# Kernel tuning notes

Hardware: AMD Instinct MI355X
Metric: run time of the kernel (lower is better)

## Reference

```python
import jax, jax.numpy as jnp
import numpy as np

B, L, R = 4, 2048, 1024        # batch, seq_len, residual_dim
HID, EXP, K = 64, 2, 3          # hidden_dim, expansion_factor, conv_kernel_size
D = HID * EXP                   # ssm_input_dim = 128
N = HID                         # SSM state size = 64


def setup_inputs() -> dict:
    key = jax.random.key(0)
    ks = jax.random.split(key, 16)
    g = lambda k, s: jax.random.normal(k, s, dtype=jnp.float32) * 0.02
    inp = {
        "up_x":   jax.random.normal(ks[0], (B, L, R), dtype=jnp.float32),
        "W_up":   g(ks[1], (R, 2 * D)),
        "b_up":   g(ks[2], (2 * D,)),
        "conv_w": g(ks[3], (D, K)),          # depthwise Conv1d weight [C,1,K] squeezed
        "conv_b": g(ks[4], (D,)),
        "W_delta": g(ks[5], (D, D)),
        "b_delta": g(ks[6], (D,)),
        "W_B":    g(ks[7], (D, N)),
        "b_B":    g(ks[8], (N,)),
        "W_C":    g(ks[9], (D, N)),
        "b_C":    g(ks[10], (N,)),
        "A_log":  jnp.log(jnp.broadcast_to(jnp.arange(1, N + 1, dtype=jnp.float32), (D, N))),
        "D_skip": jnp.ones((D,), dtype=jnp.float32),
        "W_down": g(ks[11], (D, R)),
        "b_down": g(ks[12], (R,)),
    }
    return inp


def reference(up_x, W_up, b_up, conv_w, conv_b, W_delta, b_delta,
              W_B, b_B, W_C, b_C, A_log, D_skip, W_down, b_down):
    Lq = up_x.shape[1]
    u = up_x @ W_up + b_up                               # [B,L,2D]
    left, right = jnp.split(u, 2, axis=-1)               # each [B,L,D]

    # causal depthwise conv (pad left K-1, truncate to L)
    xp = jnp.pad(left, ((0, 0), (K - 1, 0), (0, 0)))     # [B,L+K-1,D]
    conv = sum(conv_w[:, k] * xp[:, k:k + Lq, :] for k in range(K)) + conv_b
    x = jax.nn.silu(conv)                                # [B,L,D]

    # S6 selective scan
    delta = jax.nn.softplus(x @ W_delta + b_delta)       # [B,L,D]
    Bm = x @ W_B + b_B                                   # [B,L,N]
    Cm = x @ W_C + b_C                                   # [B,L,N]
    A = -jnp.exp(A_log)                                  # [D,N]
    dA = jnp.exp(delta[..., None] * A)                   # [B,L,D,N]
    dBx = delta[..., None] * Bm[:, :, None, :] * x[..., None]  # [B,L,D,N]

    def step(h, inputs):
        dA_t, dBx_t, C_t = inputs                        # [B,D,N],[B,D,N],[B,N]
        h = dA_t * h + dBx_t
        y_t = jnp.einsum('bdn,bn->bd', h, C_t)
        return h, y_t

    h0 = jnp.zeros((up_x.shape[0], D, N), dtype=x.dtype)
    _, ys = jax.lax.scan(step, h0, (jnp.swapaxes(dA, 0, 1),
                                    jnp.swapaxes(dBx, 0, 1),
                                    jnp.swapaxes(Cm, 0, 1)))
    y = jnp.swapaxes(ys, 0, 1) + D_skip * x              # [B,L,D]

    gated = y * jax.nn.silu(right)                       # SiLU gate
    return gated @ W_down + b_down                       # [B,L,R]
```

## Files before the change

### kernel.cpp

```cpp
#include <hip/hip_runtime.h>
#include <math.h>

#define B_ 4
#define L_ 2048
#define R_ 1024
#define D_ 128
#define N_ 64
#define TWO_D 256
#define M_ (B_*L_)

#define LNC 6
#define NC 64

#define LSTR 68
#define LSTRX 136

typedef __attribute__((ext_vector_type(8))) short bf16x8;
typedef __attribute__((ext_vector_type(4))) float f32x4;
typedef __attribute__((ext_vector_type(4))) unsigned short u16x4;

__device__ __forceinline__ float silu_f(float z) {
    return z * __builtin_amdgcn_rcpf(1.0f + __expf(-z));
}

__device__ __forceinline__ float softplus_f(float z) {
    return fmaxf(z, 0.0f) + __logf(1.0f + __expf(-fabsf(z)));
}

__device__ __forceinline__ short f2bf(float f) {
    union { float f; unsigned int u; } v; v.f = f;
    unsigned int r = v.u + 0x7FFF + ((v.u >> 16) & 1);
    return (short)(r >> 16);
}

__device__ __forceinline__ float bf2f(unsigned short s) {
    union { float f; unsigned int u; } v;
    v.u = ((unsigned int)s) << 16;
    return v.f;
}

__device__ __forceinline__ bf16x8 pack8(float4 a, float4 b) {
    bf16x8 r;
    r[0] = f2bf(a.x); r[1] = f2bf(a.y); r[2] = f2bf(a.z); r[3] = f2bf(a.w);
    r[4] = f2bf(b.x); r[5] = f2bf(b.y); r[6] = f2bf(b.z); r[7] = f2bf(b.w);
    return r;
}

__global__ __launch_bounds__(256) void gemm_up_splitk(
    const float* __restrict__ A,
    const float* __restrict__ W,
    float* __restrict__ P0,
    float* __restrict__ P1)
{
    __shared__ short Al[128 * LSTR];
    __shared__ short Bl[64 * LSTR];

    int lid = blockIdx.x;
    int xcd = lid & 7;
    int slot = lid >> 3;
    int bm = xcd * 8 + (slot >> 3);
    int r3 = slot & 7;
    int bn = r3 & 3;
    int split = r3 >> 2;
    float* P = split ? P1 : P0;
    int k0 = split * 512;

    int tid = threadIdx.x;
    int w = tid >> 6, l = tid & 63;
    int lm = l & 15, q = l >> 4;
    int wm = w * 32;

    f32x4 acc[2][4];
    #pragma unroll
    for (int i = 0; i < 2; i++)
        #pragma unroll
        for (int f = 0; f < 4; f++)
            acc[i][f] = (f32x4){0.f, 0.f, 0.f, 0.f};

    int ar = tid >> 1, ak = (tid & 1) * 16;
    int bcol = tid & 63, bk = (tid >> 6) * 8;

    const float* Ag = A + (size_t)(bm * 128 + ar) * 1024 + k0 + ak;
    const float* Wg = W + (size_t)k0 * TWO_D + (size_t)bn * 64 + bcol;

    for (int kt = 0; kt < 512; kt += 32) {
        float4 a0 = *(const float4*)(Ag + kt);
        float4 a1 = *(const float4*)(Ag + kt + 4);
        float4 a2 = *(const float4*)(Ag + kt + 8);
        float4 a3 = *(const float4*)(Ag + kt + 12);
        *(bf16x8*)&Al[ar * LSTR + ak]     = pack8(a0, a1);
        *(bf16x8*)&Al[ar * LSTR + ak + 8] = pack8(a2, a3);

        float w0 = Wg[(size_t)(kt + bk + 0) * TWO_D];
        float w1 = Wg[(size_t)(kt + bk + 1) * TWO_D];
        float w2 = Wg[(size_t)(kt + bk + 2) * TWO_D];
        float w3 = Wg[(size_t)(kt + bk + 3) * TWO_D];
        float w4 = Wg[(size_t)(kt + bk + 4) * TWO_D];
        float w5 = Wg[(size_t)(kt + bk + 5) * TWO_D];
        float w6 = Wg[(size_t)(kt + bk + 6) * TWO_D];
        float w7 = Wg[(size_t)(kt + bk + 7) * TWO_D];
        *(bf16x8*)&Bl[bcol * LSTR + bk] =
            pack8(make_float4(w0, w1, w2, w3), make_float4(w4, w5, w6, w7));

        __syncthreads();

        bf16x8 af0 = *(bf16x8*)&Al[(wm + lm) * LSTR + q * 8];
        bf16x8 af1 = *(bf16x8*)&Al[(wm + 16 + lm) * LSTR + q * 8];
        bf16x8 bfr[4];
        #pragma unroll
        for (int f = 0; f < 4; f++)
            bfr[f] = *(bf16x8*)&Bl[(f * 16 + lm) * LSTR + q * 8];

        #pragma unroll
        for (int f = 0; f < 4; f++) {
            acc[0][f] = __builtin_amdgcn_mfma_f32_16x16x32_bf16(af0, bfr[f], acc[0][f], 0, 0, 0);
            acc[1][f] = __builtin_amdgcn_mfma_f32_16x16x32_bf16(af1, bfr[f], acc[1][f], 0, 0, 0);
        }

        __syncthreads();
    }

    #pragma unroll
    for (int i = 0; i < 2; i++)
        #pragma unroll
        for (int f = 0; f < 4; f++)
            #pragma unroll
            for (int e = 0; e < 4; e++) {
                int row = bm * 128 + wm + i * 16 + q * 4 + e;
                int col = bn * 64 + f * 16 + lm;
                P[(size_t)row * TWO_D + col] = acc[i][f][e];
            }
}

__global__ __launch_bounds__(256) void convproj_mfma(
    const float* __restrict__ P0,
    const float* __restrict__ P1,
    const float* __restrict__ b_up,
    const float* __restrict__ conv_w,
    const float* __restrict__ conv_b,
    const float* __restrict__ W_delta, const float* __restrict__ b_delta,
    const float* __restrict__ W_B,     const float* __restrict__ b_B,
    const float* __restrict__ W_C,     const float* __restrict__ b_C,
    unsigned short* __restrict__ x,
    float* __restrict__ u,
    unsigned short* __restrict__ delta,
    unsigned short* __restrict__ Bm,
    unsigned short* __restrict__ Cm)
{
    __shared__ float uu[66 * 128];
    __shared__ short Xl[64 * LSTRX];
    __shared__ short Bl[64 * LSTR];

    int lid = blockIdx.x;
    int xcd = lid & 7;
    int slot = lid >> 3;
    int bm = xcd * 16 + (slot >> 2);
    int bn = slot & 3;
    int tid = threadIdx.x;

    bool seq_start = (bm & 31) == 0;

    #pragma unroll
    for (int i = 0; i < 9; i++) {
        int fi = tid + i * 256;
        if (fi < 2112) {
            int row = fi >> 5;
            int c4 = (fi & 31) * 4;
            int gr = bm * 64 + row - 2;
            float4 v;
            if (seq_start && row < 2) {
                v = make_float4(0.f, 0.f, 0.f, 0.f);
            } else {
                size_t gi = (size_t)gr * TWO_D + c4;
                float4 p0 = *(const float4*)&P0[gi];
                float4 p1 = *(const float4*)&P1[gi];
                float4 bb = *(const float4*)&b_up[c4];
                v = make_float4(p0.x + p1.x + bb.x, p0.y + p1.y + bb.y,
                                p0.z + p1.z + bb.z, p0.w + p1.w + bb.w);
            }
            *(float4*)&uu[fi * 4] = v;
        }
    }

    if (bn == 1) {
        #pragma unroll
        for (int i = 0; i < 8; i++) {
            int fi = tid + i * 256;
            int row = fi >> 5;
            int c4 = (fi & 31) * 4 + 128;
            int gr = bm * 64 + row;
            size_t gi = (size_t)gr * TWO_D + c4;
            float4 p0 = *(const float4*)&P0[gi];
            float4 p1 = *(const float4*)&P1[gi];
            float4 bb = *(const float4*)&b_up[c4];
            *(float4*)&u[gi] = make_float4(p0.x + p1.x + bb.x, p0.y + p1.y + bb.y,
                                           p0.z + p1.z + bb.z, p0.w + p1.w + bb.w);
        }
    }
    __syncthreads();

    #pragma unroll
    for (int i = 0; i < 8; i++) {
        int fi = tid + i * 256;
        int row = fi >> 5;
        int c4 = (fi & 31) * 4;
        float4 v2 = *(const float4*)&uu[(row + 2) * 128 + c4];
        float4 v1 = *(const float4*)&uu[(row + 1) * 128 + c4];
        float4 v0 = *(const float4*)&uu[(row + 0) * 128 + c4];
        float4 z;
        {
            float w0 = conv_w[(c4 + 0) * 3 + 0], w1 = conv_w[(c4 + 0) * 3 + 1], w2 = conv_w[(c4 + 0) * 3 + 2];
            z.x = silu_f(fmaf(w0, v0.x, fmaf(w1, v1.x, fmaf(w2, v2.x, conv_b[c4 + 0]))));
        }
        {
            float w0 = conv_w[(c4 + 1) * 3 + 0], w1 = conv_w[(c4 + 1) * 3 + 1], w2 = conv_w[(c4 + 1) * 3 + 2];
            z.y = silu_f(fmaf(w0, v0.y, fmaf(w1, v1.y, fmaf(w2, v2.y, conv_b[c4 + 1]))));
        }
        {
            float w0 = conv_w[(c4 + 2) * 3 + 0], w1 = conv_w[(c4 + 2) * 3 + 1], w2 = conv_w[(c4 + 2) * 3 + 2];
            z.z = silu_f(fmaf(w0, v0.z, fmaf(w1, v1.z, fmaf(w2, v2.z, conv_b[c4 + 2]))));
        }
        {
            float w0 = conv_w[(c4 + 3) * 3 + 0], w1 = conv_w[(c4 + 3) * 3 + 1], w2 = conv_w[(c4 + 3) * 3 + 2];
            z.w = silu_f(fmaf(w0, v0.w, fmaf(w1, v1.w, fmaf(w2, v2.w, conv_b[c4 + 3]))));
        }
        short4 zb;
        zb.x = f2bf(z.x); zb.y = f2bf(z.y); zb.z = f2bf(z.z); zb.w = f2bf(z.w);
        *(short4*)&Xl[row * LSTRX + c4] = zb;
        if (bn == 0) {
            int gr = bm * 64 + row;
            *(short4*)&x[(size_t)gr * D_ + c4] = zb;
        }
    }

    const float* Wsel; const float* bsel; int wstride;
    if (bn < 2)       { Wsel = W_delta + bn * 64; bsel = b_delta + bn * 64; wstride = 128; }
    else if (bn == 2) { Wsel = W_B;               bsel = b_B;               wstride = 64;  }
    else              { Wsel = W_C;               bsel = b_C;               wstride = 64;  }

    int w = tid >> 6, l = tid & 63;
    int lm = l & 15, q = l >> 4;
    int wm = (w & 1) * 32, wn = (w >> 1) * 32;

    f32x4 acc00 = {0,0,0,0}, acc01 = {0,0,0,0}, acc10 = {0,0,0,0}, acc11 = {0,0,0,0};

    int bcol = tid & 63, bk = (tid >> 6) * 8;
    const float* Wg = Wsel + bcol;

    __syncthreads();

    for (int kt = 0; kt < 128; kt += 32) {
        float w0 = Wg[(size_t)(kt + bk + 0) * wstride];
        float w1 = Wg[(size_t)(kt + bk + 1) * wstride];
        float w2 = Wg[(size_t)(kt + bk + 2) * wstride];
        float w3 = Wg[(size_t)(kt + bk + 3) * wstride];
        float w4 = Wg[(size_t)(kt + bk + 4) * wstride];
        float w5 = Wg[(size_t)(kt + bk + 5) * wstride];
        float w6 = Wg[(size_t)(kt + bk + 6) * wstride];
        float w7 = Wg[(size_t)(kt + bk + 7) * wstride];
        *(bf16x8*)&Bl[bcol * LSTR + bk] =
            pack8(make_float4(w0, w1, w2, w3), make_float4(w4, w5, w6, w7));

        __syncthreads();

        bf16x8 af0 = *(bf16x8*)&Xl[(wm + lm) * LSTRX + kt + q * 8];
        bf16x8 af1 = *(bf16x8*)&Xl[(wm + 16 + lm) * LSTRX + kt + q * 8];
        bf16x8 bf0 = *(bf16x8*)&Bl[(wn + lm) * LSTR + q * 8];
        bf16x8 bf1 = *(bf16x8*)&Bl[(wn + 16 + lm) * LSTR + q * 8];

        acc00 = __builtin_amdgcn_mfma_f32_16x16x32_bf16(af0, bf0, acc00, 0, 0, 0);
        acc01 = __builtin_amdgcn_mfma_f32_16x16x32_bf16(af0, bf1, acc01, 0, 0, 0);
        acc10 = __builtin_amdgcn_mfma_f32_16x16x32_bf16(af1, bf0, acc10, 0, 0, 0);
        acc11 = __builtin_amdgcn_mfma_f32_16x16x32_bf16(af1, bf1, acc11, 0, 0, 0);

        __syncthreads();
    }

    #pragma unroll
    for (int i = 0; i < 4; i++) {
        int r0 = bm * 64 + wm + q * 4 + i;
        int r1 = r0 + 16;
        int c0 = wn + lm;
        int c1 = c0 + 16;
        float v00 = acc00[i] + bsel[c0];
        float v01 = acc01[i] + bsel[c1];
        float v10 = acc10[i] + bsel[c0];
        float v11 = acc11[i] + bsel[c1];
        if (bn < 2) {
            int cc0 = bn * 64 + c0, cc1 = bn * 64 + c1;
            delta[(size_t)r0 * D_ + cc0] = (unsigned short)f2bf(softplus_f(v00));
            delta[(size_t)r0 * D_ + cc1] = (unsigned short)f2bf(softplus_f(v01));
            delta[(size_t)r1 * D_ + cc0] = (unsigned short)f2bf(softplus_f(v10));
            delta[(size_t)r1 * D_ + cc1] = (unsigned short)f2bf(softplus_f(v11));
        } else if (bn == 2) {
            Bm[(size_t)r0 * N_ + c0] = (unsigned short)f2bf(v00);
            Bm[(size_t)r0 * N_ + c1] = (unsigned short)f2bf(v01);
            Bm[(size_t)r1 * N_ + c0] = (unsigned short)f2bf(v10);
            Bm[(size_t)r1 * N_ + c1] = (unsigned short)f2bf(v11);
        } else {
            Cm[(size_t)r0 * N_ + c0] = (unsigned short)f2bf(v00);
            Cm[(size_t)r0 * N_ + c1] = (unsigned short)f2bf(v01);
            Cm[(size_t)r1 * N_ + c0] = (unsigned short)f2bf(v10);
            Cm[(size_t)r1 * N_ + c1] = (unsigned short)f2bf(v11);
        }
    }
}

__global__ __launch_bounds__(256) void scan_sumA(
    const unsigned short* __restrict__ delta,
    const unsigned short* __restrict__ x,
    const unsigned short* __restrict__ Bm,
    const float* __restrict__ A_log,
    float* __restrict__ ch_aprod,
    float* __restrict__ ch_h)
{
    constexpr int TCt = L_ >> LNC;
    __shared__ unsigned short ld_d[TCt * 16];
    __shared__ unsigned short ld_x[TCt * 16];
    __shared__ unsigned short ld_b[TCt * 64];

    int blk = blockIdx.x;
    int c = blk & (NC - 1);
    int dqg = (blk >> LNC) & 7;
    int b = blk >> (LNC + 3);
    int tid = threadIdx.x;
    int wv = tid >> 6;
    int l = tid & 63;
    int g = l >> 4, j = l & 15;
    int d0 = dqg * 16;
    int d = d0 + wv * 4 + g;
    int dloc = wv * 4 + g;

    size_t row0 = (size_t)b * L_ + c * TCt;

    {
        int t = (tid & 127) >> 2;
        int c4 = (tid & 3) * 4;
        const unsigned short* src = (tid < 128) ? delta : x;
        unsigned short* dst = (tid < 128) ? ld_d : ld_x;
        *(u16x4*)&dst[t * 16 + c4] = *(const u16x4*)&src[(row0 + t) * D_ + d0 + c4];
    }
    {
        int t = tid >> 3;
        int c8 = (tid & 7) * 8;
        *(bf16x8*)&ld_b[t * 64 + c8] = *(const bf16x8*)&Bm[(row0 + t) * N_ + c8];
    }

    const float LOG2E = 1.44269504089f;
    float4 Ar = *(const float4*)&A_log[d * N_ + j * 4];
    float Ai0 = -__expf(Ar.x) * LOG2E;
    float Ai1 = -__expf(Ar.y) * LOG2E;
    float Ai2 = -__expf(Ar.z) * LOG2E;
    float Ai3 = -__expf(Ar.w) * LOG2E;

    __syncthreads();

    float h0 = 0, h1 = 0, h2 = 0, h3 = 0;
    float S = 0;

    #pragma unroll 8
    for (int t = 0; t < TCt; t++) {
        float dl = bf2f(ld_d[t * 16 + dloc]);
        float xv = bf2f(ld_x[t * 16 + dloc]);
        u16x4 bv = *(const u16x4*)&ld_b[t * 64 + j * 4];
        float e0 = exp2f(dl * Ai0);
        float e1 = exp2f(dl * Ai1);
        float e2 = exp2f(dl * Ai2);
        float e3 = exp2f(dl * Ai3);
        float dbx = dl * xv;
        h0 = fmaf(e0, h0, dbx * bf2f(bv[0]));
        h1 = fmaf(e1, h1, dbx * bf2f(bv[1]));
        h2 = fmaf(e2, h2, dbx * bf2f(bv[2]));
        h3 = fmaf(e3, h3, dbx * bf2f(bv[3]));
        S += dl;
    }

    size_t ci = (((size_t)b * D_ + d) * NC + c) * N_ + j * 4;
    *(float4*)&ch_aprod[ci] = make_float4(exp2f(Ai0 * S), exp2f(Ai1 * S),
                                          exp2f(Ai2 * S), exp2f(Ai3 * S));
    *(float4*)&ch_h[ci]     = make_float4(h0, h1, h2, h3);
}

__global__ __launch_bounds__(64) void scan_prefix(
    float* __restrict__ aprod_hin,
    const float* __restrict__ ch_h)
{
    int idx = blockIdx.x * 64 + threadIdx.x;
    int n = idx & 63;
    int rest = idx >> 6;
    size_t base = (size_t)rest * NC * N_ + n;
    float h = 0.0f;
    #pragma unroll 8
    for (int c = 0; c < NC; c++) {
        size_t o = base + (size_t)c * N_;
        float a  = aprod_hin[o];
        float hh = ch_h[o];
        aprod_hin[o] = h;
        h = fmaf(a, h, hh);
    }
}

__global__ __launch_bounds__(256) void scan_outB(
    const unsigned short* __restrict__ delta,
    const unsigned short* __restrict__ x,
    const unsigned short* __restrict__ Bm,
    const unsigned short* __restrict__ Cm,
    const float* __restrict__ A_log,
    const float* __restrict__ D_skip,
    const float* __restrict__ hin,
    const float* __restrict__ u,
    short* __restrict__ gated)
{
    constexpr int TCt = L_ >> LNC;
    __shared__ unsigned short ld_d[TCt * 16];
    __shared__ unsigned short ld_x[TCt * 16];
    __shared__ unsigned short ld_b[TCt * 64];
    __shared__ unsigned short ld_c[TCt * 64];
    __shared__ float yl[TCt * 16];

    int blk = blockIdx.x;
    int c = blk & (NC - 1);
    int dqg = (blk >> LNC) & 7;
    int b = blk >> (LNC + 3);
    int tid = threadIdx.x;
    int wv = tid >> 6;
    int l = tid & 63;
    int g = l >> 4, j = l & 15;
    int d0 = dqg * 16;
    int d = d0 + wv * 4 + g;
    int dloc = wv * 4 + g;

    size_t row0 = (size_t)b * L_ + c * TCt;

    {
        int t = (tid & 127) >> 2;
        int c4 = (tid & 3) * 4;
        const unsigned short* src = (tid < 128) ? delta : x;
        unsigned short* dst = (tid < 128) ? ld_d : ld_x;
        *(u16x4*)&dst[t * 16 + c4] = *(const u16x4*)&src[(row0 + t) * D_ + d0 + c4];
    }
    {
        int t = tid >> 3;
        int c8 = (tid & 7) * 8;
        *(bf16x8*)&ld_b[t * 64 + c8] = *(const bf16x8*)&Bm[(row0 + t) * N_ + c8];
        *(bf16x8*)&ld_c[t * 64 + c8] = *(const bf16x8*)&Cm[(row0 + t) * N_ + c8];
    }

    const float LOG2E = 1.44269504089f;
    float4 Ar = *(const float4*)&A_log[d * N_ + j * 4];
    float Ai0 = -__expf(Ar.x) * LOG2E;
    float Ai1 = -__expf(Ar.y) * LOG2E;
    float Ai2 = -__expf(Ar.z) * LOG2E;
    float Ai3 = -__expf(Ar.w) * LOG2E;
    float dsk = D_skip[d];

    float4 hv = *(const float4*)&hin[(((size_t)b * D_ + d) * NC + c) * N_ + j * 4];
    float h0 = hv.x, h1 = hv.y, h2 = hv.z, h3 = hv.w;

    __syncthreads();

    #pragma unroll 8
    for (int t = 0; t < TCt; t++) {
        float dl = bf2f(ld_d[t * 16 + dloc]);
        float xv = bf2f(ld_x[t * 16 + dloc]);
        u16x4 bv = *(const u16x4*)&ld_b[t * 64 + j * 4];
        u16x4 cv = *(const u16x4*)&ld_c[t * 64 + j * 4];
        float e0 = exp2f(dl * Ai0);
        float e1 = exp2f(dl * Ai1);
        float e2 = exp2f(dl * Ai2);
        float e3 = exp2f(dl * Ai3);
        float dbx = dl * xv;
        h0 = fmaf(e0, h0, dbx * bf2f(bv[0]));
        h1 = fmaf(e1, h1, dbx * bf2f(bv[1]));
        h2 = fmaf(e2, h2, dbx * bf2f(bv[2]));
        h3 = fmaf(e3, h3, dbx * bf2f(bv[3]));
        float p = fmaf(h0, bf2f(cv[0]), fmaf(h1, bf2f(cv[1]),
                  fmaf(h2, bf2f(cv[2]), h3 * bf2f(cv[3]))));
        p += __shfl_xor(p, 1, 64);
        p += __shfl_xor(p, 2, 64);
        p += __shfl_xor(p, 4, 64);
        p += __shfl_xor(p, 8, 64);
        if (j == 0) yl[t * 16 + dloc] = fmaf(dsk, xv, p);
    }

    __syncthreads();

    if (tid < 128) {
        int t = tid >> 2;
        int c4 = (tid & 3) * 4;
        size_t row = row0 + t;
        float4 yv = *(float4*)&yl[t * 16 + c4];
        float4 gv = *(const float4*)&u[row * TWO_D + 128 + d0 + c4];
        short4 o;
        o.x = f2bf(yv.x * silu_f(gv.x));
        o.y = f2bf(yv.y * silu_f(gv.y));
        o.z = f2bf(yv.z * silu_f(gv.z));
        o.w = f2bf(yv.w * silu_f(gv.w));
        *(short4*)&gated[row * D_ + d0 + c4] = o;
    }
}

__global__ __launch_bounds__(256) void gemm_down_mfma(
    const short* __restrict__ gated,
    const float* __restrict__ W,
    const float* __restrict__ bias,
    float* __restrict__ out)
{
    __shared__ short Al[64 * LSTR];
    __shared__ short Bl[64 * LSTR];

    int lid = blockIdx.x;
    int xcd = lid & 7;
    int slot = lid >> 3;
    int bm = xcd * 16 + (slot >> 4);
    int bn = slot & 15;

    int tid = threadIdx.x;
    int w = tid >> 6, l = tid & 63;
    int lm = l & 15, q = l >> 4;
    int wm = (w & 1) * 32, wn = (w >> 1) * 32;

    f32x4 acc00 = {0,0,0,0}, acc01 = {0,0,0,0}, acc10 = {0,0,0,0}, acc11 = {0,0,0,0};

    int ar = tid >> 2, ak = (tid & 3) * 8;
    int bcol = tid & 63, bk = (tid >> 6) * 8;

    const short* Gg = gated + (size_t)(bm * 64 + ar) * D_ + ak;
    const float* Wg = W + (size_t)bn * 64 + bcol;

    for (int kt = 0; kt < 128; kt += 32) {
        bf16x8 av = *(const bf16x8*)(Gg + kt);
        *(bf16x8*)&Al[ar * LSTR + ak] = av;

        float w0 = Wg[(size_t)(kt + bk + 0) * R_];
        float w1 = Wg[(size_t)(kt + bk + 1) * R_];
        float w2 = Wg[(size_t)(kt + bk + 2) * R_];
        float w3 = Wg[(size_t)(kt + bk + 3) * R_];
        float w4 = Wg[(size_t)(kt + bk + 4) * R_];
        float w5 = Wg[(size_t)(kt + bk + 5) * R_];
        float w6 = Wg[(size_t)(kt + bk + 6) * R_];
        float w7 = Wg[(size_t)(kt + bk + 7) * R_];
        *(bf16x8*)&Bl[bcol * LSTR + bk] =
            pack8(make_float4(w0, w1, w2, w3), make_float4(w4, w5, w6, w7));

        __syncthreads();

        bf16x8 af0 = *(bf16x8*)&Al[(wm + lm) * LSTR + q * 8];
        bf16x8 af1 = *(bf16x8*)&Al[(wm + 16 + lm) * LSTR + q * 8];
        bf16x8 bf0 = *(bf16x8*)&Bl[(wn + lm) * LSTR + q * 8];
        bf16x8 bf1 = *(bf16x8*)&Bl[(wn + 16 + lm) * LSTR + q * 8];

        acc00 = __builtin_amdgcn_mfma_f32_16x16x32_bf16(af0, bf0, acc00, 0, 0, 0);
        acc01 = __builtin_amdgcn_mfma_f32_16x16x32_bf16(af0, bf1, acc01, 0, 0, 0);
        acc10 = __builtin_amdgcn_mfma_f32_16x16x32_bf16(af1, bf0, acc10, 0, 0, 0);
        acc11 = __builtin_amdgcn_mfma_f32_16x16x32_bf16(af1, bf1, acc11, 0, 0, 0);

        __syncthreads();
    }

    #pragma unroll
    for (int i = 0; i < 4; i++) {
        int r0 = bm * 64 + wm + q * 4 + i;
        int r1 = r0 + 16;
        int c0 = bn * 64 + wn + lm;
        int c1 = c0 + 16;
        out[(size_t)r0 * R_ + c0] = acc00[i] + bias[c0];
        out[(size_t)r0 * R_ + c1] = acc01[i] + bias[c1];
        out[(size_t)r1 * R_ + c0] = acc10[i] + bias[c0];
        out[(size_t)r1 * R_ + c1] = acc11[i] + bias[c1];
    }
}

extern "C" void kernel_launch(void* const* d_in, const int* in_sizes, int n_in,
                              void* d_out, int out_size, void* d_ws, size_t ws_size,
                              hipStream_t stream)
{
    const float* up_x    = (const float*)d_in[0];
    const float* W_up    = (const float*)d_in[1];
    const float* b_up    = (const float*)d_in[2];
    const float* conv_w  = (const float*)d_in[3];
    const float* conv_b  = (const float*)d_in[4];
    const float* W_delta = (const float*)d_in[5];
    const float* b_delta = (const float*)d_in[6];
    const float* W_B     = (const float*)d_in[7];
    const float* b_B     = (const float*)d_in[8];
    const float* W_C     = (const float*)d_in[9];
    const float* b_C     = (const float*)d_in[10];
    const float* A_log   = (const float*)d_in[11];
    const float* D_skip  = (const float*)d_in[12];
    const float* W_down  = (const float*)d_in[13];
    const float* b_down  = (const float*)d_in[14];

    float* out = (float*)d_out;
    float* ws  = (float*)d_ws;

    float* u = ws;
    unsigned short* x16     = (unsigned short*)(u + (size_t)M_ * TWO_D);
    unsigned short* delta16 = x16     + (size_t)M_ * D_;
    unsigned short* Bm16    = delta16 + (size_t)M_ * D_;
    unsigned short* Cm16    = Bm16    + (size_t)M_ * N_;
    unsigned short* gated   = Cm16    + (size_t)M_ * N_;
    float* ch_aprod = (float*)(gated + (size_t)M_ * D_);
    float* ch_h     = ch_aprod + (size_t)B_ * D_ * NC * N_;
    float* P0       = ch_h     + (size_t)B_ * D_ * NC * N_;
    float* P1       = P0       + (size_t)M_ * TWO_D;

    gemm_up_splitk<<<512, 256, 0, stream>>>(up_x, W_up, P0, P1);

    convproj_mfma<<<512, 256, 0, stream>>>(
        P0, P1, b_up, conv_w, conv_b,
        W_delta, b_delta, W_B, b_B, W_C, b_C,
        x16, u, delta16, Bm16, Cm16);

    scan_sumA<<<B_ * 8 * NC, 256, 0, stream>>>(
        delta16, x16, Bm16, A_log, ch_aprod, ch_h);
    scan_prefix<<<(B_ * D_ * N_) / 64, 64, 0, stream>>>(
        ch_aprod, ch_h);
    scan_outB<<<B_ * 8 * NC, 256, 0, stream>>>(
        delta16, x16, Bm16, Cm16, A_log, D_skip, ch_aprod, u, (short*)gated);

    gemm_down_mfma<<<2048, 256, 0, stream>>>(
        (const short*)gated, W_down, b_down, out);
}
```

Baseline: 202.6 us.

## Pre-transpose weights to bf16 and load MFMA B fragments directly from global

Adds a prep kernel that converts W_up, W_down, W_delta, W_B and W_C to bf16 in transposed (N-major) layout once per call. The three GEMM kernels then read B fragments straight from global memory instead of doing strided fp32 loads, converting and staging through LDS. The down GEMM also reads its A operand directly from global, which removes all LDS use and barriers there. This cuts per-block strided weight loads and syncs, at the cost of an extra launch, extra workspace, and uncoalesced 16-byte fragment loads that depend on L2 hits.

```diff
diff --git a/kernel.cpp b/kernel.cpp
--- a/kernel.cpp
+++ b/kernel.cpp
@@ -46,14 +46,69 @@
     return r;
 }
 
+__global__ __launch_bounds__(256) void prep_weights(
+    const float* __restrict__ W_up,
+    const float* __restrict__ W_down,
+    const float* __restrict__ W_delta,
+    const float* __restrict__ W_B,
+    const float* __restrict__ W_C,
+    unsigned short* __restrict__ WupT,
+    unsigned short* __restrict__ WdownT,
+    unsigned short* __restrict__ WdT,
+    unsigned short* __restrict__ WbT,
+    unsigned short* __restrict__ WcT)
+{
+    int blk = blockIdx.x, tid = threadIdx.x;
+    if (blk < 256) {
+        int fi = blk * 256 + tid;
+        int k = fi >> 6, n4 = (fi & 63) * 4;
+        float4 v = *(const float4*)&W_up[(size_t)k * 256 + n4];
+        WupT[(size_t)(n4 + 0) * 1024 + k] = (unsigned short)f2bf(v.x);
+        WupT[(size_t)(n4 + 1) * 1024 + k] = (unsigned short)f2bf(v.y);
+        WupT[(size_t)(n4 + 2) * 1024 + k] = (unsigned short)f2bf(v.z);
+        WupT[(size_t)(n4 + 3) * 1024 + k] = (unsigned short)f2bf(v.w);
+    } else if (blk < 384) {
+        int fi = (blk - 256) * 256 + tid;
+        int k = fi >> 8, n4 = (fi & 255) * 4;
+        float4 v = *(const float4*)&W_down[(size_t)k * 1024 + n4];
+        WdownT[(size_t)(n4 + 0) * 128 + k] = (unsigned short)f2bf(v.x);
+        WdownT[(size_t)(n4 + 1) * 128 + k] = (unsigned short)f2bf(v.y);
+        WdownT[(size_t)(n4 + 2) * 128 + k] = (unsigned short)f2bf(v.z);
+        WdownT[(size_t)(n4 + 3) * 128 + k] = (unsigned short)f2bf(v.w);
+    } else if (blk < 400) {
+        int fi = (blk - 384) * 256 + tid;
+        int k = fi >> 5, n4 = (fi & 31) * 4;
+        float4 v = *(const float4*)&W_delta[(size_t)k * 128 + n4];
+        WdT[(size_t)(n4 + 0) * 128 + k] = (unsigned short)f2bf(v.x);
+        WdT[(size_t)(n4 + 1) * 128 + k] = (unsigned short)f2bf(v.y);
+        WdT[(size_t)(n4 + 2) * 128 + k] = (unsigned short)f2bf(v.z);
+        WdT[(size_t)(n4 + 3) * 128 + k] = (unsigned short)f2bf(v.w);
+    } else if (blk < 408) {
+        int fi = (blk - 400) * 256 + tid;
+        int k = fi >> 4, n4 = (fi & 15) * 4;
+        float4 v = *(const float4*)&W_B[(size_t)k * 64 + n4];
+        WbT[(size_t)(n4 + 0) * 128 + k] = (unsigned short)f2bf(v.x);
+        WbT[(size_t)(n4 + 1) * 128 + k] = (unsigned short)f2bf(v.y);
+        WbT[(size_t)(n4 + 2) * 128 + k] = (unsigned short)f2bf(v.z);
+        WbT[(size_t)(n4 + 3) * 128 + k] = (unsigned short)f2bf(v.w);
+    } else {
+        int fi = (blk - 408) * 256 + tid;
+        int k = fi >> 4, n4 = (fi & 15) * 4;
+        float4 v = *(const float4*)&W_C[(size_t)k * 64 + n4];
+        WcT[(size_t)(n4 + 0) * 128 + k] = (unsigned short)f2bf(v.x);
+        WcT[(size_t)(n4 + 1) * 128 + k] = (unsigned short)f2bf(v.y);
+        WcT[(size_t)(n4 + 2) * 128 + k] = (unsigned short)f2bf(v.z);
+        WcT[(size_t)(n4 + 3) * 128 + k] = (unsigned short)f2bf(v.w);
+    }
+}
+
 __global__ __launch_bounds__(256) void gemm_up_splitk(
     const float* __restrict__ A,
-    const float* __restrict__ W,
+    const unsigned short* __restrict__ WupT,
     float* __restrict__ P0,
     float* __restrict__ P1)
 {
     __shared__ short Al[128 * LSTR];
-    __shared__ short Bl[64 * LSTR];
 
     int lid = blockIdx.x;
     int xcd = lid & 7;
@@ -78,10 +133,9 @@
             acc[i][f] = (f32x4){0.f, 0.f, 0.f, 0.f};
 
     int ar = tid >> 1, ak = (tid & 1) * 16;
-    int bcol = tid & 63, bk = (tid >> 6) * 8;
 
     const float* Ag = A + (size_t)(bm * 128 + ar) * 1024 + k0 + ak;
-    const float* Wg = W + (size_t)k0 * TWO_D + (size_t)bn * 64 + bcol;
+    const unsigned short* Wb = WupT + (size_t)(bn * 64 + lm) * 1024 + k0 + q * 8;
 
     for (int kt = 0; kt < 512; kt += 32) {
         float4 a0 = *(const float4*)(Ag + kt);
@@ -91,25 +145,15 @@
         *(bf16x8*)&Al[ar * LSTR + ak]     = pack8(a0, a1);
         *(bf16x8*)&Al[ar * LSTR + ak + 8] = pack8(a2, a3);
 
-        float w0 = Wg[(size_t)(kt + bk + 0) * TWO_D];
-        float w1 = Wg[(size_t)(kt + bk + 1) * TWO_D];
-        float w2 = Wg[(size_t)(kt + bk + 2) * TWO_D];
-        float w3 = Wg[(size_t)(kt + bk + 3) * TWO_D];
-        float w4 = Wg[(size_t)(kt + bk + 4) * TWO_D];
-        float w5 = Wg[(size_t)(kt + bk + 5) * TWO_D];
-        float w6 = Wg[(size_t)(kt + bk + 6) * TWO_D];
-        float w7 = Wg[(size_t)(kt + bk + 7) * TWO_D];
-        *(bf16x8*)&Bl[bcol * LSTR + bk] =
-            pack8(make_float4(w0, w1, w2, w3), make_float4(w4, w5, w6, w7));
-
-        __syncthreads();
-
-        bf16x8 af0 = *(bf16x8*)&Al[(wm + lm) * LSTR + q * 8];
-        bf16x8 af1 = *(bf16x8*)&Al[(wm + 16 + lm) * LSTR + q * 8];
         bf16x8 bfr[4];
         #pragma unroll
         for (int f = 0; f < 4; f++)
-            bfr[f] = *(bf16x8*)&Bl[(f * 16 + lm) * LSTR + q * 8];
+            bfr[f] = *(const bf16x8*)(Wb + (size_t)f * 16 * 1024 + kt);
+
+        __syncthreads();
+
+        bf16x8 af0 = *(bf16x8*)&Al[(wm + lm) * LSTR + q * 8];
+        bf16x8 af1 = *(bf16x8*)&Al[(wm + 16 + lm) * LSTR + q * 8];
 
         #pragma unroll
         for (int f = 0; f < 4; f++) {
@@ -138,9 +182,12 @@
     const float* __restrict__ b_up,
     const float* __restrict__ conv_w,
     const float* __restrict__ conv_b,
-    const float* __restrict__ W_delta, const float* __restrict__ b_delta,
-    const float* __restrict__ W_B,     const float* __restrict__ b_B,
-    const float* __restrict__ W_C,     const float* __restrict__ b_C,
+    const unsigned short* __restrict__ WdT,
+    const float* __restrict__ b_delta,
+    const unsigned short* __restrict__ WbT,
+    const float* __restrict__ b_B,
+    const unsigned short* __restrict__ WcT,
+    const float* __restrict__ b_C,
     unsigned short* __restrict__ x,
     float* __restrict__ u,
     unsigned short* __restrict__ delta,
@@ -149,7 +196,6 @@
 {
     __shared__ float uu[66 * 128];
     __shared__ short Xl[64 * LSTRX];
-    __shared__ short Bl[64 * LSTR];
 
     int lid = blockIdx.x;
     int xcd = lid & 7;
@@ -233,10 +279,10 @@
         }
     }
 
-    const float* Wsel; const float* bsel; int wstride;
-    if (bn < 2)       { Wsel = W_delta + bn * 64; bsel = b_delta + bn * 64; wstride = 128; }
-    else if (bn == 2) { Wsel = W_B;               bsel = b_B;               wstride = 64;  }
-    else              { Wsel = W_C;               bsel = b_C;               wstride = 64;  }
+    const unsigned short* WT; const float* bsel;
+    if (bn < 2)       { WT = WdT + (size_t)bn * 64 * 128; bsel = b_delta + bn * 64; }
+    else if (bn == 2) { WT = WbT;                          bsel = b_B; }
+    else              { WT = WcT;                          bsel = b_C; }
 
     int w = tid >> 6, l = tid & 63;
     int lm = l & 15, q = l >> 4;
@@ -244,36 +290,22 @@
 
     f32x4 acc00 = {0,0,0,0}, acc01 = {0,0,0,0}, acc10 = {0,0,0,0}, acc11 = {0,0,0,0};
 
-    int bcol = tid & 63, bk = (tid >> 6) * 8;
-    const float* Wg = Wsel + bcol;
+    const unsigned short* Wf0 = WT + (size_t)(wn + lm) * 128 + q * 8;
+    const unsigned short* Wf1 = Wf0 + (size_t)16 * 128;
 
     __syncthreads();
 
+    #pragma unroll
     for (int kt = 0; kt < 128; kt += 32) {
-        float w0 = Wg[(size_t)(kt + bk + 0) * wstride];
-        float w1 = Wg[(size_t)(kt + bk + 1) * wstride];
-        float w2 = Wg[(size_t)(kt + bk + 2) * wstride];
-        float w3 = Wg[(size_t)(kt + bk + 3) * wstride];
-        float w4 = Wg[(size_t)(kt + bk + 4) * wstride];
-        float w5 = Wg[(size_t)(kt + bk + 5) * wstride];
-        float w6 = Wg[(size_t)(kt + bk + 6) * wstride];
-        float w7 = Wg[(size_t)(kt + bk + 7) * wstride];
-        *(bf16x8*)&Bl[bcol * LSTR + bk] =
-            pack8(make_float4(w0, w1, w2, w3), make_float4(w4, w5, w6, w7));
-
-        __syncthreads();
-
+        bf16x8 bf0 = *(const bf16x8*)(Wf0 + kt);
+        bf16x8 bf1 = *(const bf16x8*)(Wf1 + kt);
         bf16x8 af0 = *(bf16x8*)&Xl[(wm + lm) * LSTRX + kt + q * 8];
         bf16x8 af1 = *(bf16x8*)&Xl[(wm + 16 + lm) * LSTRX + kt + q * 8];
-        bf16x8 bf0 = *(bf16x8*)&Bl[(wn + lm) * LSTR + q * 8];
-        bf16x8 bf1 = *(bf16x8*)&Bl[(wn + 16 + lm) * LSTR + q * 8];
 
         acc00 = __builtin_amdgcn_mfma_f32_16x16x32_bf16(af0, bf0, acc00, 0, 0, 0);
         acc01 = __builtin_amdgcn_mfma_f32_16x16x32_bf16(af0, bf1, acc01, 0, 0, 0);
         acc10 = __builtin_amdgcn_mfma_f32_16x16x32_bf16(af1, bf0, acc10, 0, 0, 0);
         acc11 = __builtin_amdgcn_mfma_f32_16x16x32_bf16(af1, bf1, acc11, 0, 0, 0);
-
-        __syncthreads();
     }
 
     #pragma unroll
@@ -502,13 +534,10 @@
 
 __global__ __launch_bounds__(256) void gemm_down_mfma(
     const short* __restrict__ gated,
-    const float* __restrict__ W,
+    const unsigned short* __restrict__ WdownT,
     const float* __restrict__ bias,
     float* __restrict__ out)
 {
-    __shared__ short Al[64 * LSTR];
-    __shared__ short Bl[64 * LSTR];
-
     int lid = blockIdx.x;
     int xcd = lid & 7;
     int slot = lid >> 3;
@@ -522,40 +551,20 @@
 
     f32x4 acc00 = {0,0,0,0}, acc01 = {0,0,0,0}, acc10 = {0,0,0,0}, acc11 = {0,0,0,0};
 
-    int ar = tid >> 2, ak = (tid & 3) * 8;
-    int bcol = tid & 63, bk = (tid >> 6) * 8;
-
-    const short* Gg = gated + (size_t)(bm * 64 + ar) * D_ + ak;
-    const float* Wg = W + (size_t)bn * 64 + bcol;
-
+    const short* Ga = gated + (size_t)(bm * 64 + wm + lm) * D_ + q * 8;
+    const unsigned short* Wb = WdownT + (size_t)(bn * 64 + wn + lm) * 128 + q * 8;
+
+    #pragma unroll
     for (int kt = 0; kt < 128; kt += 32) {
-        bf16x8 av = *(const bf16x8*)(Gg + kt);
-        *(bf16x8*)&Al[ar * LSTR + ak] = av;
-
-        float w0 = Wg[(size_t)(kt + bk + 0) * R_];
-        float w1 = Wg[(size_t)(kt + bk + 1) * R_];
-        float w2 = Wg[(size_t)(kt + bk + 2) * R_];
-        float w3 = Wg[(size_t)(kt + bk + 3) * R_];
-        float w4 = Wg[(size_t)(kt + bk + 4) * R_];
-        float w5 = Wg[(size_t)(kt + bk + 5) * R_];
-        float w6 = Wg[(size_t)(kt + bk + 6) * R_];
-        float w7 = Wg[(size_t)(kt + bk + 7) * R_];
-        *(bf16x8*)&Bl[bcol * LSTR + bk] =
-            pack8(make_float4(w0, w1, w2, w3), make_float4(w4, w5, w6, w7));
-
-        __syncthreads();
-
-        bf16x8 af0 = *(bf16x8*)&Al[(wm + lm) * LSTR + q * 8];
-        bf16x8 af1 = *(bf16x8*)&Al[(wm + 16 + lm) * LSTR + q * 8];
-        bf16x8 bf0 = *(bf16x8*)&Bl[(wn + lm) * LSTR + q * 8];
-        bf16x8 bf1 = *(bf16x8*)&Bl[(wn + 16 + lm) * LSTR + q * 8];
+        bf16x8 af0 = *(const bf16x8*)(Ga + kt);
+        bf16x8 af1 = *(const bf16x8*)(Ga + (size_t)16 * D_ + kt);
+        bf16x8 bf0 = *(const bf16x8*)(Wb + kt);
+        bf16x8 bf1 = *(const bf16x8*)(Wb + (size_t)16 * 128 + kt);
 
         acc00 = __builtin_amdgcn_mfma_f32_16x16x32_bf16(af0, bf0, acc00, 0, 0, 0);
         acc01 = __builtin_amdgcn_mfma_f32_16x16x32_bf16(af0, bf1, acc01, 0, 0, 0);
         acc10 = __builtin_amdgcn_mfma_f32_16x16x32_bf16(af1, bf0, acc10, 0, 0, 0);
         acc11 = __builtin_amdgcn_mfma_f32_16x16x32_bf16(af1, bf1, acc11, 0, 0, 0);
-
-        __syncthreads();
     }
 
     #pragma unroll
@@ -604,12 +613,20 @@
     float* ch_h     = ch_aprod + (size_t)B_ * D_ * NC * N_;
     float* P0       = ch_h     + (size_t)B_ * D_ * NC * N_;
     float* P1       = P0       + (size_t)M_ * TWO_D;
-
-    gemm_up_splitk<<<512, 256, 0, stream>>>(up_x, W_up, P0, P1);
+    unsigned short* WupT   = (unsigned short*)(P1 + (size_t)M_ * TWO_D);
+    unsigned short* WdownT = WupT   + (size_t)256 * 1024;
+    unsigned short* WdT    = WdownT + (size_t)1024 * 128;
+    unsigned short* WbT    = WdT    + (size_t)128 * 128;
+    unsigned short* WcT    = WbT    + (size_t)64 * 128;
+
+    prep_weights<<<416, 256, 0, stream>>>(
+        W_up, W_down, W_delta, W_B, W_C, WupT, WdownT, WdT, WbT, WcT);
+
+    gemm_up_splitk<<<512, 256, 0, stream>>>(up_x, WupT, P0, P1);
 
     convproj_mfma<<<512, 256, 0, stream>>>(
         P0, P1, b_up, conv_w, conv_b,
-        W_delta, b_delta, W_B, b_B, W_C, b_C,
+        WdT, b_delta, WbT, b_B, WcT, b_C,
         x16, u, delta16, Bm16, Cm16);
 
     scan_sumA<<<B_ * 8 * NC, 256, 0, stream>>>(
@@ -620,5 +637,5 @@
         delta16, x16, Bm16, Cm16, A_log, D_skip, ch_aprod, u, (short*)gated);
 
     gemm_down_mfma<<<2048, 256, 0, stream>>>(
-        (const short*)gated, W_down, b_down, out);
-}
+        (const short*)gated, WdownT, b_down, out);
+}
```

New measurement: 216.8 us. +7.0%, slower.

## Double-buffer up-projection GEMM and stage full K tiles in small GEMMs

Applied to the files above, without the earlier changes.

The up-projection GEMM now uses double-buffered shared tiles with K step 64. Global loads for the next tile are issued before the MFMAs on the current one, and one barrier per iteration is dropped. In the conv-projection and down-projection kernels the whole K=128 weight (and activation) tile is loaded once into shared memory, with weight loads hoisted ahead of the conv stage. This removes per-step barriers and lets global latency overlap computation. The cost is more registers and more shared memory, which may lower occupancy.

```diff
diff --git a/kernel.cpp b/kernel.cpp
--- a/kernel.cpp
+++ b/kernel.cpp
@@ -52,8 +52,8 @@
     float* __restrict__ P0,
     float* __restrict__ P1)
 {
-    __shared__ short Al[128 * LSTR];
-    __shared__ short Bl[64 * LSTR];
+    __shared__ short Al[2][128 * LSTR];
+    __shared__ short Bl[2][64 * LSTR];
 
     int lid = blockIdx.x;
     int xcd = lid & 7;
@@ -77,47 +77,55 @@
         for (int f = 0; f < 4; f++)
             acc[i][f] = (f32x4){0.f, 0.f, 0.f, 0.f};
 
-    int ar = tid >> 1, ak = (tid & 1) * 16;
-    int bcol = tid & 63, bk = (tid >> 6) * 8;
+    int ar = tid >> 1, ak = (tid & 1) * 32;
+    int bcol = tid & 63, bk = (tid >> 6) * 16;
 
     const float* Ag = A + (size_t)(bm * 128 + ar) * 1024 + k0 + ak;
     const float* Wg = W + (size_t)k0 * TWO_D + (size_t)bn * 64 + bcol;
 
-    for (int kt = 0; kt < 512; kt += 32) {
-        float4 a0 = *(const float4*)(Ag + kt);
-        float4 a1 = *(const float4*)(Ag + kt + 4);
-        float4 a2 = *(const float4*)(Ag + kt + 8);
-        float4 a3 = *(const float4*)(Ag + kt + 12);
-        *(bf16x8*)&Al[ar * LSTR + ak]     = pack8(a0, a1);
-        *(bf16x8*)&Al[ar * LSTR + ak + 8] = pack8(a2, a3);
-
-        float w0 = Wg[(size_t)(kt + bk + 0) * TWO_D];
-        float w1 = Wg[(size_t)(kt + bk + 1) * TWO_D];
-        float w2 = Wg[(size_t)(kt + bk + 2) * TWO_D];
-        float w3 = Wg[(size_t)(kt + bk + 3) * TWO_D];
-        float w4 = Wg[(size_t)(kt + bk + 4) * TWO_D];
-        float w5 = Wg[(size_t)(kt + bk + 5) * TWO_D];
-        float w6 = Wg[(size_t)(kt + bk + 6) * TWO_D];
-        float w7 = Wg[(size_t)(kt + bk + 7) * TWO_D];
-        *(bf16x8*)&Bl[bcol * LSTR + bk] =
-            pack8(make_float4(w0, w1, w2, w3), make_float4(w4, w5, w6, w7));
+    float4 a[8];
+    float wv[16];
+    #pragma unroll
+    for (int i = 0; i < 8; i++) a[i] = *(const float4*)(Ag + i * 4);
+    #pragma unroll
+    for (int i = 0; i < 16; i++) wv[i] = Wg[(size_t)(bk + i) * TWO_D];
+
+    int p = 0;
+    for (int kt = 0; kt < 512; kt += 64) {
+        #pragma unroll
+        for (int i = 0; i < 4; i++)
+            *(bf16x8*)&Al[p][ar * LSTR + ak + i * 8] = pack8(a[2 * i], a[2 * i + 1]);
+        *(bf16x8*)&Bl[p][bcol * LSTR + bk] =
+            pack8(make_float4(wv[0], wv[1], wv[2], wv[3]),
+                  make_float4(wv[4], wv[5], wv[6], wv[7]));
+        *(bf16x8*)&Bl[p][bcol * LSTR + bk + 8] =
+            pack8(make_float4(wv[8], wv[9], wv[10], wv[11]),
+                  make_float4(wv[12], wv[13], wv[14], wv[15]));
+
+        if (kt + 64 < 512) {
+            #pragma unroll
+            for (int i = 0; i < 8; i++)
+                a[i] = *(const float4*)(Ag + kt + 64 + i * 4);
+            #pragma unroll
+            for (int i = 0; i < 16; i++)
+                wv[i] = Wg[(size_t)(kt + 64 + bk + i) * TWO_D];
+        }
 
         __syncthreads();
 
-        bf16x8 af0 = *(bf16x8*)&Al[(wm + lm) * LSTR + q * 8];
-        bf16x8 af1 = *(bf16x8*)&Al[(wm + 16 + lm) * LSTR + q * 8];
-        bf16x8 bfr[4];
         #pragma unroll
-        for (int f = 0; f < 4; f++)
-            bfr[f] = *(bf16x8*)&Bl[(f * 16 + lm) * LSTR + q * 8];
-
-        #pragma unroll
-        for (int f = 0; f < 4; f++) {
-            acc[0][f] = __builtin_amdgcn_mfma_f32_16x16x32_bf16(af0, bfr[f], acc[0][f], 0, 0, 0);
-            acc[1][f] = __builtin_amdgcn_mfma_f32_16x16x32_bf16(af1, bfr[f], acc[1][f], 0, 0, 0);
-        }
-
-        __syncthreads();
+        for (int kk = 0; kk < 2; kk++) {
+            bf16x8 af0 = *(bf16x8*)&Al[p][(wm + lm) * LSTR + kk * 32 + q * 8];
+            bf16x8 af1 = *(bf16x8*)&Al[p][(wm + 16 + lm) * LSTR + kk * 32 + q * 8];
+            #pragma unroll
+            for (int f = 0; f < 4; f++) {
+                bf16x8 bfr = *(bf16x8*)&Bl[p][(f * 16 + lm) * LSTR + kk * 32 + q * 8];
+                acc[0][f] = __builtin_amdgcn_mfma_f32_16x16x32_bf16(af0, bfr, acc[0][f], 0, 0, 0);
+                acc[1][f] = __builtin_amdgcn_mfma_f32_16x16x32_bf16(af1, bfr, acc[1][f], 0, 0, 0);
+            }
+        }
+
+        p ^= 1;
     }
 
     #pragma unroll
@@ -149,7 +157,7 @@
 {
     __shared__ float uu[66 * 128];
     __shared__ short Xl[64 * LSTRX];
-    __shared__ short Bl[64 * LSTR];
+    __shared__ short Bl[64 * LSTRX];
 
     int lid = blockIdx.x;
     int xcd = lid & 7;
@@ -197,6 +205,18 @@
                                            p0.z + p1.z + bb.z, p0.w + p1.w + bb.w);
         }
     }
+
+    const float* Wsel; const float* bsel; int wstride;
+    if (bn < 2)       { Wsel = W_delta + bn * 64; bsel = b_delta + bn * 64; wstride = 128; }
+    else if (bn == 2) { Wsel = W_B;               bsel = b_B;               wstride = 64;  }
+    else              { Wsel = W_C;               bsel = b_C;               wstride = 64;  }
+
+    int bcol = tid & 63, kb = (tid >> 6) * 32;
+    const float* Wg = Wsel + bcol;
+    float wv[32];
+    #pragma unroll
+    for (int i = 0; i < 32; i++) wv[i] = Wg[(size_t)(kb + i) * wstride];
+
     __syncthreads();
 
     #pragma unroll
@@ -233,10 +253,11 @@
         }
     }
 
-    const float* Wsel; const float* bsel; int wstride;
-    if (bn < 2)       { Wsel = W_delta + bn * 64; bsel = b_delta + bn * 64; wstride = 128; }
-    else if (bn == 2) { Wsel = W_B;               bsel = b_B;               wstride = 64;  }
-    else              { Wsel = W_C;               bsel = b_C;               wstride = 64;  }
+    #pragma unroll
+    for (int j = 0; j < 4; j++)
+        *(bf16x8*)&Bl[bcol * LSTRX + kb + j * 8] =
+            pack8(make_float4(wv[8 * j + 0], wv[8 * j + 1], wv[8 * j + 2], wv[8 * j + 3]),
+                  make_float4(wv[8 * j + 4], wv[8 * j + 5], wv[8 * j + 6], wv[8 * j + 7]));
 
     int w = tid >> 6, l = tid & 63;
     int lm = l & 15, q = l >> 4;
@@ -244,36 +265,19 @@
 
     f32x4 acc00 = {0,0,0,0}, acc01 = {0,0,0,0}, acc10 = {0,0,0,0}, acc11 = {0,0,0,0};
 
-    int bcol = tid & 63, bk = (tid >> 6) * 8;
-    const float* Wg = Wsel + bcol;
-
     __syncthreads();
 
+    #pragma unroll
     for (int kt = 0; kt < 128; kt += 32) {
-        float w0 = Wg[(size_t)(kt + bk + 0) * wstride];
-        float w1 = Wg[(size_t)(kt + bk + 1) * wstride];
-        float w2 = Wg[(size_t)(kt + bk + 2) * wstride];
-        float w3 = Wg[(size_t)(kt + bk + 3) * wstride];
-        float w4 = Wg[(size_t)(kt + bk + 4) * wstride];
-        float w5 = Wg[(size_t)(kt + bk + 5) * wstride];
-        float w6 = Wg[(size_t)(kt + bk + 6) * wstride];
-        float w7 = Wg[(size_t)(kt + bk + 7) * wstride];
-        *(bf16x8*)&Bl[bcol * LSTR + bk] =
-            pack8(make_float4(w0, w1, w2, w3), make_float4(w4, w5, w6, w7));
-
-        __syncthreads();
-
         bf16x8 af0 = *(bf16x8*)&Xl[(wm + lm) * LSTRX + kt + q * 8];
         bf16x8 af1 = *(bf16x8*)&Xl[(wm + 16 + lm) * LSTRX + kt + q * 8];
-        bf16x8 bf0 = *(bf16x8*)&Bl[(wn + lm) * LSTR + q * 8];
-        bf16x8 bf1 = *(bf16x8*)&Bl[(wn + 16 + lm) * LSTR + q * 8];
+        bf16x8 bf0 = *(bf16x8*)&Bl[(wn + lm) * LSTRX + kt + q * 8];
+        bf16x8 bf1 = *(bf16x8*)&Bl[(wn + 16 + lm) * LSTRX + kt + q * 8];
 
         acc00 = __builtin_amdgcn_mfma_f32_16x16x32_bf16(af0, bf0, acc00, 0, 0, 0);
         acc01 = __builtin_amdgcn_mfma_f32_16x16x32_bf16(af0, bf1, acc01, 0, 0, 0);
         acc10 = __builtin_amdgcn_mfma_f32_16x16x32_bf16(af1, bf0, acc10, 0, 0, 0);
         acc11 = __builtin_amdgcn_mfma_f32_16x16x32_bf16(af1, bf1, acc11, 0, 0, 0);
-
-        __syncthreads();
     }
 
     #pragma unroll
@@ -506,8 +510,8 @@
     const float* __restrict__ bias,
     float* __restrict__ out)
 {
-    __shared__ short Al[64 * LSTR];
-    __shared__ short Bl[64 * LSTR];
+    __shared__ short Al[64 * LSTRX];
+    __shared__ short Bl[64 * LSTRX];
 
     int lid = blockIdx.x;
     int xcd = lid & 7;
@@ -522,40 +526,41 @@
 
     f32x4 acc00 = {0,0,0,0}, acc01 = {0,0,0,0}, acc10 = {0,0,0,0}, acc11 = {0,0,0,0};
 
-    int ar = tid >> 2, ak = (tid & 3) * 8;
-    int bcol = tid & 63, bk = (tid >> 6) * 8;
+    int ar = tid >> 2, ak = (tid & 3) * 32;
+    int bcol = tid & 63, kb = (tid >> 6) * 32;
 
     const short* Gg = gated + (size_t)(bm * 64 + ar) * D_ + ak;
     const float* Wg = W + (size_t)bn * 64 + bcol;
 
+    bf16x8 av[4];
+    #pragma unroll
+    for (int jj = 0; jj < 4; jj++) av[jj] = *(const bf16x8*)(Gg + jj * 8);
+    float wvr[32];
+    #pragma unroll
+    for (int i = 0; i < 32; i++) wvr[i] = Wg[(size_t)(kb + i) * R_];
+
+    #pragma unroll
+    for (int jj = 0; jj < 4; jj++)
+        *(bf16x8*)&Al[ar * LSTRX + ak + jj * 8] = av[jj];
+    #pragma unroll
+    for (int jj = 0; jj < 4; jj++)
+        *(bf16x8*)&Bl[bcol * LSTRX + kb + jj * 8] =
+            pack8(make_float4(wvr[8 * jj + 0], wvr[8 * jj + 1], wvr[8 * jj + 2], wvr[8 * jj + 3]),
+                  make_float4(wvr[8 * jj + 4], wvr[8 * jj + 5], wvr[8 * jj + 6], wvr[8 * jj + 7]));
+
+    __syncthreads();
+
+    #pragma unroll
     for (int kt = 0; kt < 128; kt += 32) {
-        bf16x8 av = *(const bf16x8*)(Gg + kt);
-        *(bf16x8*)&Al[ar * LSTR + ak] = av;
-
-        float w0 = Wg[(size_t)(kt + bk + 0) * R_];
-        float w1 = Wg[(size_t)(kt + bk + 1) * R_];
-        float w2 = Wg[(size_t)(kt + bk + 2) * R_];
-        float w3 = Wg[(size_t)(kt + bk + 3) * R_];
-        float w4 = Wg[(size_t)(kt + bk + 4) * R_];
-        float w5 = Wg[(size_t)(kt + bk + 5) * R_];
-        float w6 = Wg[(size_t)(kt + bk + 6) * R_];
-        float w7 = Wg[(size_t)(kt + bk + 7) * R_];
-        *(bf16x8*)&Bl[bcol * LSTR + bk] =
-            pack8(make_float4(w0, w1, w2, w3), make_float4(w4, w5, w6, w7));
-
-        __syncthreads();
-
-        bf16x8 af0 = *(bf16x8*)&Al[(wm + lm) * LSTR + q * 8];
-        bf16x8 af1 = *(bf16x8*)&Al[(wm + 16 + lm) * LSTR + q * 8];
-        bf16x8 bf0 = *(bf16x8*)&Bl[(wn + lm) * LSTR + q * 8];
-        bf16x8 bf1 = *(bf16x8*)&Bl[(wn + 16 + lm) * LSTR + q * 8];
+        bf16x8 af0 = *(bf16x8*)&Al[(wm + lm) * LSTRX + kt + q * 8];
+        bf16x8 af1 = *(bf16x8*)&Al[(wm + 16 + lm) * LSTRX + kt + q * 8];
+        bf16x8 bf0 = *(bf16x8*)&Bl[(wn + lm) * LSTRX + kt + q * 8];
+        bf16x8 bf1 = *(bf16x8*)&Bl[(wn + 16 + lm) * LSTRX + kt + q * 8];
 
         acc00 = __builtin_amdgcn_mfma_f32_16x16x32_bf16(af0, bf0, acc00, 0, 0, 0);
         acc01 = __builtin_amdgcn_mfma_f32_16x16x32_bf16(af0, bf1, acc01, 0, 0, 0);
         acc10 = __builtin_amdgcn_mfma_f32_16x16x32_bf16(af1, bf0, acc10, 0, 0, 0);
         acc11 = __builtin_amdgcn_mfma_f32_16x16x32_bf16(af1, bf1, acc11, 0, 0, 0);
-
-        __syncthreads();
     }
 
     #pragma unroll
```

Result: faster. 197.9 us (-2.3%).
